# Kernel tuning notes

Measured on AMD Instinct MI355X. Metric: run time of the kernel, lower is better.

## Reference

```python
import jax, jax.numpy as jnp
import numpy as np

V, E, H = 32000, 512, 1024  # vocab, embedding, hidden
B, T = 16, 256


def setup_inputs() -> dict:
    key = jax.random.key(0)
    ks = jax.random.split(key, 7)
    x = jax.random.randint(ks[0], (B, T), 0, V)
    emb = jax.random.normal(ks[1], (V, E), dtype=jnp.float32) * 0.02
    # Keras LSTMCell params: kernel [E,4H], recurrent_kernel [H,4H], bias [4H]
    kernel = jax.random.normal(ks[2], (E, 4 * H), dtype=jnp.float32) * (1.0 / np.sqrt(E))
    rec_kernel = jax.random.normal(ks[3], (H, 4 * H), dtype=jnp.float32) * (1.0 / np.sqrt(H))
    # unit_forget_bias: forget-gate bias initialized to 1 (gate order i,f,c,o)
    bias = jnp.concatenate([jnp.zeros(H), jnp.ones(H), jnp.zeros(2 * H)]).astype(jnp.float32)
    w_out = jax.random.normal(ks[4], (H, V), dtype=jnp.float32) * (1.0 / np.sqrt(H))
    b_out = jnp.zeros((V,), dtype=jnp.float32)
    return {"x": x, "emb": emb, "kernel": kernel, "rec_kernel": rec_kernel,
            "bias": bias, "w_out": w_out, "b_out": b_out}


def _lstm_scan(e, kernel, rec_kernel, bias):
    # e: [B, T, E] -> h_seq [B, T, H]
    Bsz = e.shape[0]
    Hs = rec_kernel.shape[0]
    # Precompute input projections for all timesteps (one big GEMM)
    zx = jnp.einsum('bte,ef->btf', e, kernel) + bias  # [B, T, 4H]
    zx_t = jnp.transpose(zx, (1, 0, 2))  # [T, B, 4H]

    def step(carry, zxt):
        h, c = carry
        z = zxt + h @ rec_kernel  # [B, 4H]
        i, f, g, o = jnp.split(z, 4, axis=-1)  # Keras gate order: i, f, c(g), o
        i = jax.nn.sigmoid(i)
        f = jax.nn.sigmoid(f)
        g = jnp.tanh(g)
        o = jax.nn.sigmoid(o)
        c = f * c + i * g
        h = o * jnp.tanh(c)
        return (h, c), h

    h0 = jnp.zeros((Bsz, Hs), dtype=e.dtype)
    c0 = jnp.zeros((Bsz, Hs), dtype=e.dtype)
    _, h_seq = jax.lax.scan(step, (h0, c0), zx_t)  # [T, B, H]
    return jnp.transpose(h_seq, (1, 0, 2))  # [B, T, H]


def reference(x, emb, kernel, rec_kernel, bias, w_out, b_out):
    e = emb[x]  # [B, T, E] embedding lookup
    h = _lstm_scan(e, kernel, rec_kernel, bias)  # [B, T, H]
    logits = jnp.einsum('bth,hv->btv', h, w_out) + b_out  # [B, T, V]
    return logits
```

## Files before the change

kernel.cpp:

```cpp
#include <hip/hip_runtime.h>
#include <cstdint>
#include <cstddef>

#define DEV __device__ __forceinline__

typedef __attribute__((ext_vector_type(4))) float f32x4;
typedef __attribute__((ext_vector_type(8))) short s16x8;
typedef __attribute__((ext_vector_type(4))) unsigned u32x4;

DEV uint16_t f2bf(float x){
  union { float f; uint32_t u; } v; v.f = x;
  uint32_t r = v.u + 0x7FFFu + ((v.u >> 16) & 1u);
  return (uint16_t)(r >> 16);
}
DEV float bf2f(uint16_t h){
  union { uint32_t u; float f; } v; v.u = ((uint32_t)h) << 16; return v.f;
}
DEV void split2(float x, uint16_t &hi, uint16_t &lo){
  hi = f2bf(x); lo = f2bf(x - bf2f(hi));
}

DEV f32x4 mfma16(s16x8 a, s16x8 b, f32x4 c){
  return __builtin_amdgcn_mfma_f32_16x16x32_bf16(a, b, c, 0, 0, 0);
}

DEV void g2l16(const void* g, void* l){
  __builtin_amdgcn_global_load_lds(
      (const __attribute__((address_space(1))) unsigned int*)g,
      (__attribute__((address_space(3))) unsigned int*)l, 16, 0, 0);
}

DEV s16x8 ldg_coh(const uint16_t* p){
  s16x8 r;
  asm volatile("global_load_dwordx4 %0, %1, off sc0 sc1" : "=v"(r) : "v"(p));
  return r;
}
DEV void stg_coh64(uint16_t* p, unsigned long long v){
  asm volatile("global_store_dwordx2 %0, %1, off sc0 sc1"
               :: "v"(p), "v"(v) : "memory");
}
DEV void stg_coh32(unsigned* p, unsigned v){
  asm volatile("global_store_dword %0, %1, off sc0 sc1"
               :: "v"(p), "v"(v) : "memory");
}
DEV u32x4 ldg_coh_u4(const unsigned* p){
  u32x4 r;
  asm volatile("global_load_dwordx4 %0, %1, off sc0 sc1\n\t"
               "s_waitcnt vmcnt(0)"
               : "=v"(r) : "v"(p) : "memory");
  return r;
}
DEV unsigned ldg_coh_u1(const unsigned* p){
  unsigned v;
  asm volatile("global_load_dword %0, %1, off sc0 sc1\n\t"
               "s_waitcnt vmcnt(0)"
               : "=v"(v) : "v"(p) : "memory");
  return v;
}

__global__ void zero_u32(unsigned* __restrict__ p){ p[threadIdx.x] = 0u; }

__global__ __launch_bounds__(256) void gather_split(
    const int* __restrict__ x, const float* __restrict__ emb,
    uint16_t* __restrict__ ehi, uint16_t* __restrict__ elo){
  int idx = blockIdx.x * 256 + threadIdx.x;
  int r = idx >> 7, k4 = idx & 127;
  int row = x[r];
  float4 v = ((const float4*)(emb + (size_t)row * 512))[k4];
  ushort4 hi, lo;
  split2(v.x, hi.x, lo.x);
  split2(v.y, hi.y, lo.y);
  split2(v.z, hi.z, lo.z);
  split2(v.w, hi.w, lo.w);
  ((ushort4*)ehi)[idx] = hi;
  ((ushort4*)elo)[idx] = lo;
}

__global__ __launch_bounds__(256) void transpose_split(
    const float* __restrict__ in, uint16_t* __restrict__ ohi,
    uint16_t* __restrict__ olo, int R, int Cc){
  __shared__ float tile[32][33];
  const int tx = threadIdx.x & 31, ty = threadIdx.x >> 5;
  const int c0 = blockIdx.x << 5, r0 = blockIdx.y << 5;
  for (int i = 0; i < 32; i += 8)
    tile[ty + i][tx] = in[(size_t)(r0 + ty + i) * Cc + c0 + tx];
  __syncthreads();
  for (int i = 0; i < 32; i += 8){
    float v = tile[tx][ty + i];
    uint16_t hi, lo; split2(v, hi, lo);
    size_t o = (size_t)(c0 + ty + i) * R + r0 + tx;
    ohi[o] = hi; olo[o] = lo;
  }
}

__global__ __launch_bounds__(256) void pack_wr(
    const float* __restrict__ wr, uint16_t* __restrict__ phi, uint16_t* __restrict__ plo){
  int t = blockIdx.x * 256 + threadIdx.x;
  int lane = t & 63, kb = (t >> 6) & 31, ntile = t >> 11;
  int q = lane >> 4, ln = lane & 15;
  int n = ((ln >> 2) << 10) + (ntile << 2) + (ln & 3);
  int k0 = (kb << 5) + (q << 3);
  union { s16x8 v; uint16_t e[8]; } uh, ul;
  for (int j = 0; j < 8; j++)
    split2(wr[(size_t)(k0 + j) * 4096 + n], uh.e[j], ul.e[j]);
  ((s16x8*)phi)[t] = uh.v;
  ((s16x8*)plo)[t] = ul.v;
}

__global__ __launch_bounds__(256) void gemm_split(
    const uint16_t* __restrict__ Ahi, const uint16_t* __restrict__ Alo,
    const uint16_t* __restrict__ Bhi, const uint16_t* __restrict__ Blo,
    const float* __restrict__ bias, float* __restrict__ C,
    int Mm, int Nn, int Kk, int rowperm){
  __shared__ __attribute__((aligned(16))) uint16_t sAhi[2][128 * 32];
  __shared__ __attribute__((aligned(16))) uint16_t sAlo[2][128 * 32];
  __shared__ __attribute__((aligned(16))) uint16_t sBhi[2][128 * 32];
  __shared__ __attribute__((aligned(16))) uint16_t sBlo[2][128 * 32];

  const int tid = threadIdx.x;
  const int lane = tid & 63, wid = tid >> 6;
  const int wm = (wid & 1) * 64, wn = (wid >> 1) * 64;
  const int q = lane >> 4, lm = lane & 15;

  const int gm = Mm >> 7, gn = Nn >> 7;
  const int GROUP = 10;
  const int per = gm * GROUP;
  const int gi = blockIdx.x / per;
  const int rem = blockIdx.x - gi * per;
  const int n0g = gi * GROUP;
  int gw = gn - n0g; if (gw > GROUP) gw = GROUP;
  const int mt = rem / gw;
  const int nt = n0g + rem % gw;
  const int m0 = mt << 7, n0 = nt << 7;

  const int row0 = tid >> 2;
  const int csw  = (tid & 3) ^ ((row0 + (row0 >> 2)) & 3);
  const size_t aoff0 = (size_t)(m0 + row0) * Kk + csw * 8;
  const size_t aoff1 = (size_t)(m0 + row0 + 64) * Kk + csw * 8;
  const size_t boff0 = (size_t)(n0 + row0) * Kk + csw * 8;
  const size_t boff1 = (size_t)(n0 + row0 + 64) * Kk + csw * 8;

  const int qs8 = ((q ^ ((lm + (lm >> 2)) & 3)) * 8);

  auto STAGE = [&](int b, int ks){
    g2l16(Ahi + aoff0 + ks, sAhi[b] + tid * 8);
    g2l16(Ahi + aoff1 + ks, sAhi[b] + 2048 + tid * 8);
    g2l16(Alo + aoff0 + ks, sAlo[b] + tid * 8);
    g2l16(Alo + aoff1 + ks, sAlo[b] + 2048 + tid * 8);
    g2l16(Bhi + boff0 + ks, sBhi[b] + tid * 8);
    g2l16(Bhi + boff1 + ks, sBhi[b] + 2048 + tid * 8);
    g2l16(Blo + boff0 + ks, sBlo[b] + tid * 8);
    g2l16(Blo + boff1 + ks, sBlo[b] + 2048 + tid * 8);
  };

  f32x4 acc[4][4];
  for (int i = 0; i < 4; i++) for (int j = 0; j < 4; j++)
    acc[i][j] = (f32x4){0.f, 0.f, 0.f, 0.f};

  STAGE(0, 0);
  __syncthreads();

  int buf = 0;
  for (int ks = 0; ks < Kk; ks += 32){
    if (ks + 32 < Kk) STAGE(buf ^ 1, ks + 32);

    const uint16_t* pAh = sAhi[buf];
    const uint16_t* pAl = sAlo[buf];
    const uint16_t* pBh = sBhi[buf];
    const uint16_t* pBl = sBlo[buf];

    s16x8 bh[4], bl[4];
    for (int j = 0; j < 4; j++){
      bh[j] = *(const s16x8*)&pBh[(wn + j * 16 + lm) * 32 + qs8];
      bl[j] = *(const s16x8*)&pBl[(wn + j * 16 + lm) * 32 + qs8];
    }
    for (int i = 0; i < 4; i++){
      s16x8 ah = *(const s16x8*)&pAh[(wm + i * 16 + lm) * 32 + qs8];
      s16x8 al = *(const s16x8*)&pAl[(wm + i * 16 + lm) * 32 + qs8];
      for (int j = 0; j < 4; j++){
        acc[i][j] = mfma16(ah, bh[j], acc[i][j]);
        acc[i][j] = mfma16(ah, bl[j], acc[i][j]);
        acc[i][j] = mfma16(al, bh[j], acc[i][j]);
      }
    }
    __syncthreads();
    buf ^= 1;
  }

  for (int i = 0; i < 4; i++){
    const int rowg = m0 + wm + i * 16 + q * 4;
    for (int j = 0; j < 4; j++){
      const int colg = n0 + wn + j * 16 + lm;
      const float bv = bias[colg];
      for (int r = 0; r < 4; r++){
        int rg = rowg + r;
        if (rowperm) rg = ((rg & 15) << 8) | (rg >> 4);
        C[(size_t)rg * Nn + colg] = acc[i][j][r] + bv;
      }
    }
  }
}

struct SMemRec {
  uint16_t Wh[32 * 64 * 8];
  uint16_t Wl[32 * 64 * 8];
  float zbuf[4][16][17];
};
struct SMemGw {
  uint16_t Ah[2][4096];
  uint16_t Al[2][4096];
  uint16_t Bh[2][4096];
  uint16_t Bl[2][4096];
};
union SMemU { SMemRec rec; SMemGw gw; };

__global__ __launch_bounds__(256, 2) void lstm_fused(
    const uint16_t* __restrict__ wphi, const uint16_t* __restrict__ wplo,
    const float* __restrict__ zx,
    uint16_t* __restrict__ hrot_hi, uint16_t* __restrict__ hrot_lo,
    uint16_t* __restrict__ h0hi, uint16_t* __restrict__ h0lo,
    uint16_t* __restrict__ h1hi, uint16_t* __restrict__ h1lo,
    unsigned* __restrict__ flags, unsigned* __restrict__ epoch,
    const uint16_t* __restrict__ wothi, const uint16_t* __restrict__ wotlo,
    const float* __restrict__ bo, float* __restrict__ out){
  __shared__ __attribute__((aligned(16))) SMemU sm;

  const int tid = threadIdx.x, lane = tid & 63, w = tid >> 6;
  const int blk = blockIdx.x;

  if (blk >= 256){
    const int wb = blk - 256;
    const int wid = tid >> 6;
    const int wm = (wid & 1) * 64, wn = (wid >> 1) * 64;
    const int q = lane >> 4, lm = lane & 15;
    const int row0 = tid >> 2;
    const int csw = (tid & 3) ^ ((row0 + (row0 >> 2)) & 3);
    const int qs8 = ((q ^ ((lm + (lm >> 2)) & 3)) * 8);
    const unsigned* ep = epoch + (wb & 7) * 32;

    for (int idx = wb; idx < 8000; idx += 256){
      const int mt = idx / 250, nt = idx - mt * 250;
      const unsigned need = (unsigned)(mt * 8 + 8);
      for (;;){
        if (ldg_coh_u1(ep) >= need) break;
        __builtin_amdgcn_s_sleep(2);
      }
      __builtin_amdgcn_sched_barrier(0);

      const int m0 = mt << 7, n0 = nt << 7;
      const size_t aoff0 = (size_t)(m0 + row0) * 1024 + csw * 8;
      const size_t aoff1 = (size_t)(m0 + row0 + 64) * 1024 + csw * 8;
      const size_t boff0 = (size_t)(n0 + row0) * 1024 + csw * 8;
      const size_t boff1 = (size_t)(n0 + row0 + 64) * 1024 + csw * 8;

      auto STAGEW = [&](int b, int ks){
        g2l16(hrot_hi + aoff0 + ks, &sm.gw.Ah[b][tid * 8]);
        g2l16(hrot_hi + aoff1 + ks, &sm.gw.Ah[b][2048 + tid * 8]);
        g2l16(hrot_lo + aoff0 + ks, &sm.gw.Al[b][tid * 8]);
        g2l16(hrot_lo + aoff1 + ks, &sm.gw.Al[b][2048 + tid * 8]);
        g2l16(wothi + boff0 + ks, &sm.gw.Bh[b][tid * 8]);
        g2l16(wothi + boff1 + ks, &sm.gw.Bh[b][2048 + tid * 8]);
        g2l16(wotlo + boff0 + ks, &sm.gw.Bl[b][tid * 8]);
        g2l16(wotlo + boff1 + ks, &sm.gw.Bl[b][2048 + tid * 8]);
      };

      f32x4 acc[4][4];
#pragma unroll
      for (int i = 0; i < 4; i++)
#pragma unroll
        for (int j = 0; j < 4; j++)
          acc[i][j] = (f32x4){0.f, 0.f, 0.f, 0.f};

      STAGEW(0, 0);
      __syncthreads();
      int buf = 0;
      for (int ks = 0; ks < 1024; ks += 32){
        if (ks + 32 < 1024) STAGEW(buf ^ 1, ks + 32);
        const uint16_t* pAh = sm.gw.Ah[buf];
        const uint16_t* pAl = sm.gw.Al[buf];
        const uint16_t* pBh = sm.gw.Bh[buf];
        const uint16_t* pBl = sm.gw.Bl[buf];
        s16x8 bh[4], bl[4];
#pragma unroll
        for (int j = 0; j < 4; j++){
          bh[j] = *(const s16x8*)&pBh[(wn + j * 16 + lm) * 32 + qs8];
          bl[j] = *(const s16x8*)&pBl[(wn + j * 16 + lm) * 32 + qs8];
        }
#pragma unroll
        for (int i = 0; i < 4; i++){
          s16x8 ah = *(const s16x8*)&pAh[(wm + i * 16 + lm) * 32 + qs8];
          s16x8 al = *(const s16x8*)&pAl[(wm + i * 16 + lm) * 32 + qs8];
#pragma unroll
          for (int j = 0; j < 4; j++){
            acc[i][j] = mfma16(ah, bh[j], acc[i][j]);
            acc[i][j] = mfma16(ah, bl[j], acc[i][j]);
            acc[i][j] = mfma16(al, bh[j], acc[i][j]);
          }
        }
        __syncthreads();
        buf ^= 1;
      }

      for (int i = 0; i < 4; i++){
        const int rowg = m0 + wm + i * 16 + q * 4;
        for (int j = 0; j < 4; j++){
          const int colg = n0 + wn + j * 16 + lm;
          const float bv = bo[colg];
          for (int r = 0; r < 4; r++){
            int rg = rowg + r;
            rg = ((rg & 15) << 8) | (rg >> 4);
            out[(size_t)rg * 32000 + colg] = acc[i][j][r] + bv;
          }
        }
      }
    }
    return;
  }

  const int q = lane >> 4, lm = lane & 15;
  const int kq = w;
  const bool is_master = (blk == 0 && w == 0);

  {
    const uint16_t* gh = wphi + (size_t)blk * 16384;
    const uint16_t* gl = wplo + (size_t)blk * 16384;
#pragma unroll
    for (int i = 0; i < 8; i++){
      const int o = (i * 256 + tid) * 8;
      g2l16(gh + o, sm.rec.Wh + o);
      g2l16(gl + o, sm.rec.Wl + o);
    }
    asm volatile("s_waitcnt vmcnt(0)" ::: "memory");
  }
  __syncthreads();

  const int aoffbase = lm * 1024 + kq * 256 + q * 8;
  const int boffbase = kq * 8 * 512 + lane * 8;

  const int tb = tid >> 2, ccin = tid & 3;
  const int thcol = blk * 4 + ccin;
  const unsigned* epoll = epoch + (blk & 7) * 32;
  float cval = 0.f;

  for (int t = 0; t < 256; t++){
    float zr0 = 0.f, zr1 = 0.f, zr2 = 0.f, zr3 = 0.f;
    if (tid < 64){
      const float* zr = zx + ((size_t)tb * 256 + t) * 4096 + thcol;
      zr0 = zr[0]; zr1 = zr[1024]; zr2 = zr[2048]; zr3 = zr[3072];
    }

    f32x4 a0 = (f32x4){0.f,0.f,0.f,0.f};
    f32x4 a1 = (f32x4){0.f,0.f,0.f,0.f};
    f32x4 a2 = (f32x4){0.f,0.f,0.f,0.f};
    if (t > 0){
      if (!is_master){
        const unsigned gen = (unsigned)t;
        for (;;){
          if (ldg_coh_u1(epoll) >= gen) break;
          __builtin_amdgcn_s_sleep(1);
        }
      }
      __builtin_amdgcn_sched_barrier(0);

      const uint16_t* hih = (t & 1) ? h1hi : h0hi;
      const uint16_t* hil = (t & 1) ? h1lo : h0lo;
      const uint16_t* ah_p = hih + aoffbase;
      const uint16_t* al_p = hil + aoffbase;
      s16x8 Ah[8], Al[8];
#pragma unroll
      for (int kb = 0; kb < 8; kb++){
        Ah[kb] = ldg_coh(ah_p + kb * 32);
        Al[kb] = ldg_coh(al_p + kb * 32);
      }
      asm volatile("s_waitcnt vmcnt(0)" ::: "memory");
      __builtin_amdgcn_sched_barrier(0);
#pragma unroll
      for (int kb = 0; kb < 8; kb++){
        s16x8 bh = *(const s16x8*)&sm.rec.Wh[boffbase + kb * 512];
        s16x8 bl = *(const s16x8*)&sm.rec.Wl[boffbase + kb * 512];
        a0 = mfma16(Ah[kb], bh, a0);
        a1 = mfma16(Ah[kb], bl, a1);
        a2 = mfma16(Al[kb], bh, a2);
      }
    }
    f32x4 acc = a0 + a1 + a2;

#pragma unroll
    for (int r = 0; r < 4; r++)
      sm.rec.zbuf[w][q * 4 + r][lm] = acc[r];
    __syncthreads();

    if (tid < 64){
      float z0 = sm.rec.zbuf[0][tb][0 * 4 + ccin] + sm.rec.zbuf[1][tb][0 * 4 + ccin]
               + sm.rec.zbuf[2][tb][0 * 4 + ccin] + sm.rec.zbuf[3][tb][0 * 4 + ccin] + zr0;
      float z1 = sm.rec.zbuf[0][tb][1 * 4 + ccin] + sm.rec.zbuf[1][tb][1 * 4 + ccin]
               + sm.rec.zbuf[2][tb][1 * 4 + ccin] + sm.rec.zbuf[3][tb][1 * 4 + ccin] + zr1;
      float z2 = sm.rec.zbuf[0][tb][2 * 4 + ccin] + sm.rec.zbuf[1][tb][2 * 4 + ccin]
               + sm.rec.zbuf[2][tb][2 * 4 + ccin] + sm.rec.zbuf[3][tb][2 * 4 + ccin] + zr2;
      float z3 = sm.rec.zbuf[0][tb][3 * 4 + ccin] + sm.rec.zbuf[1][tb][3 * 4 + ccin]
               + sm.rec.zbuf[2][tb][3 * 4 + ccin] + sm.rec.zbuf[3][tb][3 * 4 + ccin] + zr3;
      float ig = 1.f / (1.f + __expf(-z0));
      float fg = 1.f / (1.f + __expf(-z1));
      float gg = 1.f - 2.f / (__expf(2.f * z2) + 1.f);
      float og = 1.f / (1.f + __expf(-z3));
      cval = fg * cval + ig * gg;
      float h = og * (1.f - 2.f / (__expf(2.f * cval) + 1.f));
      uint16_t hh, hl; split2(h, hh, hl);

      unsigned pk = (unsigned)hh | ((unsigned)hl << 16);
      unsigned p1 = __shfl_down(pk, 1);
      unsigned p2 = __shfl_down(pk, 2);
      unsigned p3 = __shfl_down(pk, 3);
      if (ccin == 0){
        union { unsigned u32[2]; unsigned long long u64; } vhi, vlo;
        vhi.u32[0] = (pk & 0xFFFFu) | ((p1 & 0xFFFFu) << 16);
        vhi.u32[1] = (p2 & 0xFFFFu) | ((p3 & 0xFFFFu) << 16);
        vlo.u32[0] = (pk >> 16) | (p1 & 0xFFFF0000u);
        vlo.u32[1] = (p2 >> 16) | (p3 & 0xFFFF0000u);
        uint16_t* ohh = ((t & 1) ? h0hi : h1hi) + tb * 1024 + blk * 4;
        uint16_t* ohl = ((t & 1) ? h0lo : h1lo) + tb * 1024 + blk * 4;
        stg_coh64(ohh, vhi.u64);
        stg_coh64(ohl, vlo.u64);
        uint16_t* rh = hrot_hi + ((size_t)(t * 16 + tb)) * 1024 + blk * 4;
        uint16_t* rl = hrot_lo + ((size_t)(t * 16 + tb)) * 1024 + blk * 4;
        stg_coh64(rh, vhi.u64);
        stg_coh64(rl, vlo.u64);
      }
      asm volatile("s_waitcnt vmcnt(0)" ::: "memory");
      if (tid == 0)
        stg_coh32(flags + blk, (unsigned)(t + 1));
    }

    if (is_master && t < 255){
      const unsigned gen = (unsigned)(t + 1);
      for (;;){
        u32x4 f = ldg_coh_u4(flags + lane * 4);
        if (__all(f.x >= gen && f.y >= gen && f.z >= gen && f.w >= gen)) break;
        __builtin_amdgcn_s_sleep(1);
      }
      if (lane < 8)
        stg_coh32(epoch + lane * 32, gen);
    }
  }

  if (is_master){
    const unsigned gen = 256u;
    for (;;){
      u32x4 f = ldg_coh_u4(flags + lane * 4);
      if (__all(f.x >= gen && f.y >= gen && f.z >= gen && f.w >= gen)) break;
      __builtin_amdgcn_s_sleep(1);
    }
    if (lane < 8)
      stg_coh32(epoch + lane * 32, gen);
  }
}

extern "C" void kernel_launch(void* const* d_in, const int* in_sizes, int n_in,
                              void* d_out, int out_size, void* d_ws, size_t ws_size,
                              hipStream_t stream){
  (void)in_sizes; (void)n_in; (void)out_size; (void)ws_size;
  const int*   x    = (const int*)d_in[0];
  const float* emb  = (const float*)d_in[1];
  const float* wk   = (const float*)d_in[2];
  const float* wr   = (const float*)d_in[3];
  const float* bias = (const float*)d_in[4];
  const float* wo   = (const float*)d_in[5];
  const float* bo   = (const float*)d_in[6];
  float* out = (float*)d_out;

  char* w = (char*)d_ws;
  float*    zx    = (float*)w;    w += (size_t)4096 * 4096 * 4;
  uint16_t* ehi   = (uint16_t*)w; w += (size_t)4096 * 512 * 2;
  uint16_t* elo   = (uint16_t*)w; w += (size_t)4096 * 512 * 2;
  uint16_t* kthi  = (uint16_t*)w; w += (size_t)4096 * 512 * 2;
  uint16_t* ktlo  = (uint16_t*)w; w += (size_t)4096 * 512 * 2;
  uint16_t* wphi  = (uint16_t*)w; w += (size_t)1024 * 4096 * 2;
  uint16_t* wplo  = (uint16_t*)w; w += (size_t)1024 * 4096 * 2;
  uint16_t* wothi = (uint16_t*)w; w += (size_t)32000 * 1024 * 2;
  uint16_t* wotlo = (uint16_t*)w; w += (size_t)32000 * 1024 * 2;
  uint16_t* hroth = (uint16_t*)w; w += (size_t)4096 * 1024 * 2;
  uint16_t* hrotl = (uint16_t*)w; w += (size_t)4096 * 1024 * 2;
  uint16_t* h0hi  = (uint16_t*)w; w += (size_t)16 * 1024 * 2;
  uint16_t* h0lo  = (uint16_t*)w; w += (size_t)16 * 1024 * 2;
  uint16_t* h1hi  = (uint16_t*)w; w += (size_t)16 * 1024 * 2;
  uint16_t* h1lo  = (uint16_t*)w; w += (size_t)16 * 1024 * 2;
  unsigned* flags = (unsigned*)w; w += 256 * 4;
  unsigned* epoch = (unsigned*)w; w += 256 * 4;

  zero_u32<<<1, 512, 0, stream>>>(flags);
  gather_split<<<2048, 256, 0, stream>>>(x, emb, ehi, elo);
  transpose_split<<<dim3(128, 16), 256, 0, stream>>>(wk, kthi, ktlo, 512, 4096);
  pack_wr<<<2048, 256, 0, stream>>>(wr, wphi, wplo);
  transpose_split<<<dim3(1000, 32), 256, 0, stream>>>(wo, wothi, wotlo, 1024, 32000);

  gemm_split<<<1024, 256, 0, stream>>>(ehi, elo, kthi, ktlo, bias, zx,
                                       4096, 4096, 512, 0);

  {
    void* kargs[] = {
      (void*)&wphi, (void*)&wplo, (void*)&zx,
      (void*)&hroth, (void*)&hrotl,
      (void*)&h0hi, (void*)&h0lo, (void*)&h1hi, (void*)&h1lo,
      (void*)&flags, (void*)&epoch,
      (void*)&wothi, (void*)&wotlo, (void*)&bo, (void*)&out
    };
    hipError_t ce = hipLaunchCooperativeKernel((void*)lstm_fused, dim3(512),
                                               dim3(256), kargs, 0, stream);
    if (ce != hipSuccess){
      (void)hipLaunchCooperativeKernel((void*)lstm_fused, dim3(256),
                                       dim3(256), kargs, 0, stream);
      gemm_split<<<8000, 256, 0, stream>>>(hroth, hrotl, wothi, wotlo, bo, out,
                                           4096, 32000, 1024, 1);
    }
  }
}
```

Measured before the change: 2.300 ms.

## Use atomic ticket scheduler so recurrence blocks join output GEMM after finishing

The output-projection GEMM tiles are now handed out by a global atomic ticket counter instead of a static stride over 256 dedicated blocks. The 256 recurrence blocks, once the LSTM scan ends, also pull tiles from the same counter, so all 512 blocks share the tail GEMM work. The fallback path drops its separate gemm_split launch and relies on the same ticket loop. This adds one atomic and two block barriers per tile, and tiles may be claimed out of order relative to epoch readiness, which can cause extra spinning.

```diff
diff --git a/kernel.cpp b/kernel.cpp
--- a/kernel.cpp
+++ b/kernel.cpp
@@ -211,8 +211,107 @@
   uint16_t Al[2][4096];
   uint16_t Bh[2][4096];
   uint16_t Bl[2][4096];
+  unsigned tix;
 };
 union SMemU { SMemRec rec; SMemGw gw; };
+
+DEV void gemm_tiles(SMemGw& g, int tid, unsigned* ticket,
+                    const unsigned* ep,
+                    const uint16_t* hrot_hi, const uint16_t* hrot_lo,
+                    const uint16_t* wothi, const uint16_t* wotlo,
+                    const float* bo, float* out){
+  const int lane = tid & 63, wid = tid >> 6;
+  const int wm = (wid & 1) * 64, wn = (wid >> 1) * 64;
+  const int q = lane >> 4, lm = lane & 15;
+  const int row0 = tid >> 2;
+  const int csw = (tid & 3) ^ ((row0 + (row0 >> 2)) & 3);
+  const int qs8 = ((q ^ ((lm + (lm >> 2)) & 3)) * 8);
+
+  for (;;){
+    __syncthreads();
+    if (tid == 0)
+      g.tix = __hip_atomic_fetch_add(ticket, 1u, __ATOMIC_RELAXED,
+                                     __HIP_MEMORY_SCOPE_AGENT);
+    __syncthreads();
+    const unsigned idx = g.tix;
+    if (idx >= 8000u) return;
+    const int mt = (int)(idx / 250u), nt = (int)(idx - (unsigned)mt * 250u);
+
+    const unsigned need = (unsigned)(mt * 8 + 8);
+    for (;;){
+      if (ldg_coh_u1(ep) >= need) break;
+      __builtin_amdgcn_s_sleep(2);
+    }
+    __builtin_amdgcn_sched_barrier(0);
+
+    const int m0 = mt << 7, n0 = nt << 7;
+    const size_t aoff0 = (size_t)(m0 + row0) * 1024 + csw * 8;
+    const size_t aoff1 = (size_t)(m0 + row0 + 64) * 1024 + csw * 8;
+    const size_t boff0 = (size_t)(n0 + row0) * 1024 + csw * 8;
+    const size_t boff1 = (size_t)(n0 + row0 + 64) * 1024 + csw * 8;
+
+    auto STAGEW = [&](int b, int ks){
+      g2l16(hrot_hi + aoff0 + ks, &g.Ah[b][tid * 8]);
+      g2l16(hrot_hi + aoff1 + ks, &g.Ah[b][2048 + tid * 8]);
+      g2l16(hrot_lo + aoff0 + ks, &g.Al[b][tid * 8]);
+      g2l16(hrot_lo + aoff1 + ks, &g.Al[b][2048 + tid * 8]);
+      g2l16(wothi + boff0 + ks, &g.Bh[b][tid * 8]);
+      g2l16(wothi + boff1 + ks, &g.Bh[b][2048 + tid * 8]);
+      g2l16(wotlo + boff0 + ks, &g.Bl[b][tid * 8]);
+      g2l16(wotlo + boff1 + ks, &g.Bl[b][2048 + tid * 8]);
+    };
+
+    f32x4 acc[4][4];
+#pragma unroll
+    for (int i = 0; i < 4; i++)
+#pragma unroll
+      for (int j = 0; j < 4; j++)
+        acc[i][j] = (f32x4){0.f, 0.f, 0.f, 0.f};
+
+    STAGEW(0, 0);
+    __syncthreads();
+    int buf = 0;
+    for (int ks = 0; ks < 1024; ks += 32){
+      if (ks + 32 < 1024) STAGEW(buf ^ 1, ks + 32);
+      const uint16_t* pAh = g.Ah[buf];
+      const uint16_t* pAl = g.Al[buf];
+      const uint16_t* pBh = g.Bh[buf];
+      const uint16_t* pBl = g.Bl[buf];
+      s16x8 bh[4], bl[4];
+#pragma unroll
+      for (int j = 0; j < 4; j++){
+        bh[j] = *(const s16x8*)&pBh[(wn + j * 16 + lm) * 32 + qs8];
+        bl[j] = *(const s16x8*)&pBl[(wn + j * 16 + lm) * 32 + qs8];
+      }
+#pragma unroll
+      for (int i = 0; i < 4; i++){
+        s16x8 ah = *(const s16x8*)&pAh[(wm + i * 16 + lm) * 32 + qs8];
+        s16x8 al = *(const s16x8*)&pAl[(wm + i * 16 + lm) * 32 + qs8];
+#pragma unroll
+        for (int j = 0; j < 4; j++){
+          acc[i][j] = mfma16(ah, bh[j], acc[i][j]);
+          acc[i][j] = mfma16(ah, bl[j], acc[i][j]);
+          acc[i][j] = mfma16(al, bh[j], acc[i][j]);
+        }
+      }
+      __syncthreads();
+      buf ^= 1;
+    }
+
+    for (int i = 0; i < 4; i++){
+      const int rowg = m0 + wm + i * 16 + q * 4;
+      for (int j = 0; j < 4; j++){
+        const int colg = n0 + wn + j * 16 + lm;
+        const float bv = bo[colg];
+        for (int r = 0; r < 4; r++){
+          int rg = rowg + r;
+          rg = ((rg & 15) << 8) | (rg >> 4);
+          out[(size_t)rg * 32000 + colg] = acc[i][j][r] + bv;
+        }
+      }
+    }
+  }
+}
 
 __global__ __launch_bounds__(256, 2) void lstm_fused(
     const uint16_t* __restrict__ wphi, const uint16_t* __restrict__ wplo,
@@ -222,98 +321,16 @@
     uint16_t* __restrict__ h1hi, uint16_t* __restrict__ h1lo,
     unsigned* __restrict__ flags, unsigned* __restrict__ epoch,
     const uint16_t* __restrict__ wothi, const uint16_t* __restrict__ wotlo,
-    const float* __restrict__ bo, float* __restrict__ out){
+    const float* __restrict__ bo, float* __restrict__ out,
+    unsigned* __restrict__ ticket){
   __shared__ __attribute__((aligned(16))) SMemU sm;
 
   const int tid = threadIdx.x, lane = tid & 63, w = tid >> 6;
   const int blk = blockIdx.x;
+  const unsigned* ep = epoch + (blk & 7) * 32;
 
   if (blk >= 256){
-    const int wb = blk - 256;
-    const int wid = tid >> 6;
-    const int wm = (wid & 1) * 64, wn = (wid >> 1) * 64;
-    const int q = lane >> 4, lm = lane & 15;
-    const int row0 = tid >> 2;
-    const int csw = (tid & 3) ^ ((row0 + (row0 >> 2)) & 3);
-    const int qs8 = ((q ^ ((lm + (lm >> 2)) & 3)) * 8);
-    const unsigned* ep = epoch + (wb & 7) * 32;
-
-    for (int idx = wb; idx < 8000; idx += 256){
-      const int mt = idx / 250, nt = idx - mt * 250;
-      const unsigned need = (unsigned)(mt * 8 + 8);
-      for (;;){
-        if (ldg_coh_u1(ep) >= need) break;
-        __builtin_amdgcn_s_sleep(2);
-      }
-      __builtin_amdgcn_sched_barrier(0);
-
-      const int m0 = mt << 7, n0 = nt << 7;
-      const size_t aoff0 = (size_t)(m0 + row0) * 1024 + csw * 8;
-      const size_t aoff1 = (size_t)(m0 + row0 + 64) * 1024 + csw * 8;
-      const size_t boff0 = (size_t)(n0 + row0) * 1024 + csw * 8;
-      const size_t boff1 = (size_t)(n0 + row0 + 64) * 1024 + csw * 8;
-
-      auto STAGEW = [&](int b, int ks){
-        g2l16(hrot_hi + aoff0 + ks, &sm.gw.Ah[b][tid * 8]);
-        g2l16(hrot_hi + aoff1 + ks, &sm.gw.Ah[b][2048 + tid * 8]);
-        g2l16(hrot_lo + aoff0 + ks, &sm.gw.Al[b][tid * 8]);
-        g2l16(hrot_lo + aoff1 + ks, &sm.gw.Al[b][2048 + tid * 8]);
-        g2l16(wothi + boff0 + ks, &sm.gw.Bh[b][tid * 8]);
-        g2l16(wothi + boff1 + ks, &sm.gw.Bh[b][2048 + tid * 8]);
-        g2l16(wotlo + boff0 + ks, &sm.gw.Bl[b][tid * 8]);
-        g2l16(wotlo + boff1 + ks, &sm.gw.Bl[b][2048 + tid * 8]);
-      };
-
-      f32x4 acc[4][4];
-#pragma unroll
-      for (int i = 0; i < 4; i++)
-#pragma unroll
-        for (int j = 0; j < 4; j++)
-          acc[i][j] = (f32x4){0.f, 0.f, 0.f, 0.f};
-
-      STAGEW(0, 0);
-      __syncthreads();
-      int buf = 0;
-      for (int ks = 0; ks < 1024; ks += 32){
-        if (ks + 32 < 1024) STAGEW(buf ^ 1, ks + 32);
-        const uint16_t* pAh = sm.gw.Ah[buf];
-        const uint16_t* pAl = sm.gw.Al[buf];
-        const uint16_t* pBh = sm.gw.Bh[buf];
-        const uint16_t* pBl = sm.gw.Bl[buf];
-        s16x8 bh[4], bl[4];
-#pragma unroll
-        for (int j = 0; j < 4; j++){
-          bh[j] = *(const s16x8*)&pBh[(wn + j * 16 + lm) * 32 + qs8];
-          bl[j] = *(const s16x8*)&pBl[(wn + j * 16 + lm) * 32 + qs8];
-        }
-#pragma unroll
-        for (int i = 0; i < 4; i++){
-          s16x8 ah = *(const s16x8*)&pAh[(wm + i * 16 + lm) * 32 + qs8];
-          s16x8 al = *(const s16x8*)&pAl[(wm + i * 16 + lm) * 32 + qs8];
-#pragma unroll
-          for (int j = 0; j < 4; j++){
-            acc[i][j] = mfma16(ah, bh[j], acc[i][j]);
-            acc[i][j] = mfma16(ah, bl[j], acc[i][j]);
-            acc[i][j] = mfma16(al, bh[j], acc[i][j]);
-          }
-        }
-        __syncthreads();
-        buf ^= 1;
-      }
-
-      for (int i = 0; i < 4; i++){
-        const int rowg = m0 + wm + i * 16 + q * 4;
-        for (int j = 0; j < 4; j++){
-          const int colg = n0 + wn + j * 16 + lm;
-          const float bv = bo[colg];
-          for (int r = 0; r < 4; r++){
-            int rg = rowg + r;
-            rg = ((rg & 15) << 8) | (rg >> 4);
-            out[(size_t)rg * 32000 + colg] = acc[i][j][r] + bv;
-          }
-        }
-      }
-    }
+    gemm_tiles(sm.gw, tid, ticket, ep, hrot_hi, hrot_lo, wothi, wotlo, bo, out);
     return;
   }
 
@@ -339,7 +356,6 @@
 
   const int tb = tid >> 2, ccin = tid & 3;
   const int thcol = blk * 4 + ccin;
-  const unsigned* epoll = epoch + (blk & 7) * 32;
   float cval = 0.f;
 
   for (int t = 0; t < 256; t++){
@@ -356,7 +372,7 @@
       if (!is_master){
         const unsigned gen = (unsigned)t;
         for (;;){
-          if (ldg_coh_u1(epoll) >= gen) break;
+          if (ldg_coh_u1(ep) >= gen) break;
           __builtin_amdgcn_s_sleep(1);
         }
       }
@@ -453,6 +469,8 @@
     if (lane < 8)
       stg_coh32(epoch + lane * 32, gen);
   }
+
+  gemm_tiles(sm.gw, tid, ticket, ep, hrot_hi, hrot_lo, wothi, wotlo, bo, out);
 }
 
 extern "C" void kernel_launch(void* const* d_in, const int* in_sizes, int n_in,
@@ -484,10 +502,11 @@
   uint16_t* h0lo  = (uint16_t*)w; w += (size_t)16 * 1024 * 2;
   uint16_t* h1hi  = (uint16_t*)w; w += (size_t)16 * 1024 * 2;
   uint16_t* h1lo  = (uint16_t*)w; w += (size_t)16 * 1024 * 2;
-  unsigned* flags = (unsigned*)w; w += 256 * 4;
-  unsigned* epoch = (unsigned*)w; w += 256 * 4;
-
-  zero_u32<<<1, 512, 0, stream>>>(flags);
+  unsigned* flags = (unsigned*)w; w += 1024;
+  unsigned* epoch = (unsigned*)w; w += 1024;
+  unsigned* ticket= (unsigned*)w; w += 1024;
+
+  zero_u32<<<1, 768, 0, stream>>>(flags);
   gather_split<<<2048, 256, 0, stream>>>(x, emb, ehi, elo);
   transpose_split<<<dim3(128, 16), 256, 0, stream>>>(wk, kthi, ktlo, 512, 4096);
   pack_wr<<<2048, 256, 0, stream>>>(wr, wphi, wplo);
@@ -502,15 +521,14 @@
       (void*)&hroth, (void*)&hrotl,
       (void*)&h0hi, (void*)&h0lo, (void*)&h1hi, (void*)&h1lo,
       (void*)&flags, (void*)&epoch,
-      (void*)&wothi, (void*)&wotlo, (void*)&bo, (void*)&out
+      (void*)&wothi, (void*)&wotlo, (void*)&bo, (void*)&out,
+      (void*)&ticket
     };
     hipError_t ce = hipLaunchCooperativeKernel((void*)lstm_fused, dim3(512),
                                                dim3(256), kargs, 0, stream);
     if (ce != hipSuccess){
       (void)hipLaunchCooperativeKernel((void*)lstm_fused, dim3(256),
                                        dim3(256), kargs, 0, stream);
-      gemm_split<<<8000, 256, 0, stream>>>(hroth, hrotl, wothi, wotlo, bo, out,
-                                           4096, 32000, 1024, 1);
-    }
-  }
-}
+    }
+  }
+}
```

Result: no change. 2.314 ms (+0.6%).
